# Kernel optimization log

Measured on AMD Instinct MI355X. Metric: run time of the kernel, lower is better.

## Reference

```python
import jax, jax.numpy as jnp
import numpy as np

TEMPERATURE = 0.1
EPS = 1e-12  # matches torch F.normalize default eps


def setup_inputs() -> dict:
    key = jax.random.key(0)
    k1, k2 = jax.random.split(key)
    B, D = 4096, 512
    features1 = jax.random.normal(k1, (B, D), dtype=jnp.float32)
    features2 = jax.random.normal(k2, (B, D), dtype=jnp.float32)
    return {"features1": features1, "features2": features2}


def _l2_normalize(x, axis=1):
    norm = jnp.linalg.norm(x, axis=axis, keepdims=True)
    return x / jnp.maximum(norm, EPS)


def reference(features1, features2):
    B = features1.shape[0]
    f1 = _l2_normalize(features1)
    f2 = _l2_normalize(features2)
    features = jnp.concatenate([f1, f2], axis=0)  # (2B, D)
    sim = jnp.matmul(features, features.T) / TEMPERATURE  # (2B, 2B)
    # mask self-similarity on the diagonal with -inf
    diag = jnp.eye(2 * B, dtype=bool)
    sim = jnp.where(diag, -jnp.inf, sim)
    # positive pair labels: row i pairs with i+B (first half) / i-B (second half)
    labels = jnp.concatenate([jnp.arange(B) + B, jnp.arange(B)], axis=0)
    log_probs = jax.nn.log_softmax(sim, axis=-1)  # (2B, 2B)
    nll = -jnp.take_along_axis(log_probs, labels[:, None], axis=1)[:, 0]
    return jnp.mean(nll)
```

## Files before the change

kernel.cpp:

```cpp
#include <hip/hip_runtime.h>

#define NROWS 8192
#define HALF_N 4096
#define DIM 512
#define INV_T 10.0f
#define NRB 64
#define NBLOCKS 2080

typedef __attribute__((ext_vector_type(4))) float f32x4;
typedef __attribute__((ext_vector_type(2))) long long2v;

__device__ __forceinline__ void async16(const void* g, void* l) {
  __builtin_amdgcn_global_load_lds(
      (const __attribute__((address_space(1))) unsigned int*)g,
      (__attribute__((address_space(3))) unsigned int*)l, 16, 0, 0);
}

__global__ __launch_bounds__(256) void norm_cast_k(
    const float* __restrict__ f1, const float* __restrict__ f2,
    unsigned char* __restrict__ Fa, unsigned char* __restrict__ Fb,
    float* __restrict__ rowsum, float* __restrict__ out) {
  int wave = threadIdx.x >> 6;
  int lane = threadIdx.x & 63;
  int row = blockIdx.x * 4 + wave;
  const float* src = (row < HALF_N) ? (f1 + (size_t)row * DIM)
                                    : (f2 + (size_t)(row - HALF_N) * DIM);
  const float4* p = reinterpret_cast<const float4*>(src + lane * 8);
  float4 v0 = p[0];
  float4 v1 = p[1];
  float ss = v0.x*v0.x + v0.y*v0.y + v0.z*v0.z + v0.w*v0.w
           + v1.x*v1.x + v1.y*v1.y + v1.z*v1.z + v1.w*v1.w;
  #pragma unroll
  for (int off = 1; off < 64; off <<= 1) ss += __shfl_xor(ss, off);
  float scale = 1.0f / fmaxf(sqrtf(ss), 1e-12f);
  int lo = __builtin_amdgcn_cvt_pk_fp8_f32(v0.x * scale, v0.y * scale, 0, false);
  lo = __builtin_amdgcn_cvt_pk_fp8_f32(v0.z * scale, v0.w * scale, lo, true);
  int hi = __builtin_amdgcn_cvt_pk_fp8_f32(v1.x * scale, v1.y * scale, 0, false);
  hi = __builtin_amdgcn_cvt_pk_fp8_f32(v1.z * scale, v1.w * scale, hi, true);
  int2 val = make_int2(lo, hi);
  int u = lane & 7;
  int g = lane >> 3;
  int pos = 2 * (u & 3) + (u >> 2);
  *reinterpret_cast<int2*>(Fb + (size_t)row * DIM + g * 64 + pos * 8) = val;
  int chunk = g * 4 + (u & 3);
  int slot = u >> 2;
  *reinterpret_cast<int2*>(Fa + (size_t)(row >> 4) * 8192 + chunk * 256 +
                           (row & 15) * 16 + slot * 8) = val;
  if (lane == 0) rowsum[row] = 0.0f;
  if (blockIdx.x == 0 && threadIdx.x == 0) out[0] = 0.0f;
}

__global__ __launch_bounds__(256, 3) void sym_gemm_k(
    const unsigned char* __restrict__ Fa, const unsigned char* __restrict__ Fb,
    float* __restrict__ rowsum, float* __restrict__ pairsim) {
  int bx = blockIdx.x;
  int gbx = (bx & 7) * (NBLOCKS / 8) + (bx >> 3);
  int rb = 0, rem = gbx;
  while (rem >= NRB - rb) { rem -= NRB - rb; ++rb; }
  const int cb = rb + rem;
  const int row0 = rb * 128, col0 = cb * 128;

  const int tid = threadIdx.x;
  const int wave = tid >> 6;
  const int lane = tid & 63;
  const int quad = lane >> 4;
  const int colid = lane & 15;
  const int wr0 = (wave >> 1) * 64;
  const int wc0 = (wave & 1) * 64;

  __shared__ __align__(16) unsigned char Blds[128 * 64];
  __shared__ float redrow[128];
  __shared__ float redcol[128];

  if (tid < 128) { redrow[tid] = 0.0f; redcol[tid] = 0.0f; }

  const unsigned char* srcB[2]; unsigned char* dstB[2];
  #pragma unroll
  for (int seg = 0; seg < 2; ++seg) {
    int inst = wave + seg * 4;
    int r = inst * 16 + (lane >> 2);
    int c = (lane & 3) ^ ((r >> 1) & 3);
    srcB[seg] = Fb + (size_t)(col0 + r) * DIM + c * 16;
    dstB[seg] = Blds + inst * 1024;
  }

  const unsigned char* agp[4];
  #pragma unroll
  for (int t = 0; t < 4; ++t)
    agp[t] = Fa + (size_t)((row0 + wr0 + t * 16) >> 4) * 8192 +
             quad * 256 + colid * 16;

  const unsigned char* bfp[4];
  #pragma unroll
  for (int t = 0; t < 4; ++t) {
    int rc = wc0 + t * 16 + colid;
    bfp[t] = Blds + rc * 64 + ((quad ^ ((rc >> 1) & 3)) << 4);
  }

  f32x4 acc[4][4];
  #pragma unroll
  for (int t = 0; t < 4; ++t)
    #pragma unroll
    for (int u = 0; u < 4; ++u) acc[t][u] = (f32x4){0.f, 0.f, 0.f, 0.f};

  for (int kc = 0; kc < 8; ++kc) {
    __syncthreads();
    const size_t ko = (size_t)kc * 64;
    #pragma unroll
    for (int seg = 0; seg < 2; ++seg)
      async16(srcB[seg] + ko, dstB[seg]);
    long2v af[4];
    #pragma unroll
    for (int t = 0; t < 4; ++t)
      af[t] = *reinterpret_cast<const long2v*>(agp[t] + kc * 1024);
    __syncthreads();

    long2v bf[4];
    #pragma unroll
    for (int u = 0; u < 4; ++u) bf[u] = *reinterpret_cast<const long2v*>(bfp[u]);
    #pragma unroll
    for (int s = 0; s < 2; ++s)
      #pragma unroll
      for (int t = 0; t < 4; ++t)
        #pragma unroll
        for (int u = 0; u < 4; ++u)
          acc[t][u] = __builtin_amdgcn_mfma_f32_16x16x32_fp8_fp8(
              af[t][s], bf[u][s], acc[t][u], 0, 0, 0);
  }

  float re[4][4];
  float ce[4];
  #pragma unroll
  for (int t = 0; t < 4; ++t)
    #pragma unroll
    for (int r = 0; r < 4; ++r) re[t][r] = 0.0f;
  #pragma unroll
  for (int u = 0; u < 4; ++u) ce[u] = 0.0f;

  #pragma unroll
  for (int t = 0; t < 4; ++t) {
    #pragma unroll
    for (int u = 0; u < 4; ++u) {
      f32x4 a = acc[t][u];
      const int gc = col0 + wc0 + u * 16 + colid;
      #pragma unroll
      for (int r = 0; r < 4; ++r) {
        int grow = row0 + wr0 + t * 16 + quad * 4 + r;
        float sim = a[r] * INV_T;
        float e = (gc > grow) ? __expf(sim) : 0.0f;
        re[t][r] += e;
        ce[u] += e;
        if (gc == grow + HALF_N && grow < HALF_N) {
          pairsim[grow] = sim;
          pairsim[gc] = sim;
        }
      }
    }
  }

  #pragma unroll
  for (int t = 0; t < 4; ++t)
    #pragma unroll
    for (int r = 0; r < 4; ++r) {
      float v = re[t][r];
      v += __shfl_xor(v, 1); v += __shfl_xor(v, 2);
      v += __shfl_xor(v, 4); v += __shfl_xor(v, 8);
      if (colid == 0) atomicAdd(&redrow[wr0 + t * 16 + quad * 4 + r], v);
    }
  #pragma unroll
  for (int u = 0; u < 4; ++u) {
    float v = ce[u];
    v += __shfl_xor(v, 16); v += __shfl_xor(v, 32);
    if (lane < 16) atomicAdd(&redcol[wc0 + u * 16 + colid], v);
  }
  __syncthreads();
  if (tid < 128) atomicAdd(&rowsum[row0 + tid], redrow[tid]);
  else           atomicAdd(&rowsum[col0 + tid - 128], redcol[tid - 128]);
}

__global__ __launch_bounds__(256) void finalize_k(
    const float* __restrict__ rowsum, const float* __restrict__ pairsim,
    float* __restrict__ out) {
  int i = blockIdx.x * 256 + threadIdx.x;
  float local = logf(rowsum[i]) - pairsim[i];
  #pragma unroll
  for (int off = 1; off < 64; off <<= 1) local += __shfl_xor(local, off);
  if ((threadIdx.x & 63) == 0)
    atomicAdd(out, local * (1.0f / (float)NROWS));
}

extern "C" void kernel_launch(void* const* d_in, const int* in_sizes, int n_in,
                              void* d_out, int out_size, void* d_ws, size_t ws_size,
                              hipStream_t stream) {
  const float* f1 = (const float*)d_in[0];
  const float* f2 = (const float*)d_in[1];
  unsigned char* Fa = (unsigned char*)d_ws;
  unsigned char* Fb = Fa + (size_t)NROWS * DIM;
  float* rowsum = (float*)(Fb + (size_t)NROWS * DIM);
  float* pairsim = rowsum + NROWS;
  float* out = (float*)d_out;

  norm_cast_k<<<NROWS / 4, 256, 0, stream>>>(f1, f2, Fa, Fb, rowsum, out);
  sym_gemm_k<<<NBLOCKS, 256, 0, stream>>>(Fa, Fb, rowsum, pairsim);
  finalize_k<<<NROWS / 256, 256, 0, stream>>>(rowsum, pairsim, out);
}
```

Measured before the change: 104.2 us.

## Load both GEMM operands directly from global into registers with double buffering

```diff
diff --git a/kernel.cpp b/kernel.cpp
--- a/kernel.cpp
+++ b/kernel.cpp
@@ -10,16 +10,10 @@
 typedef __attribute__((ext_vector_type(4))) float f32x4;
 typedef __attribute__((ext_vector_type(2))) long long2v;
 
-__device__ __forceinline__ void async16(const void* g, void* l) {
-  __builtin_amdgcn_global_load_lds(
-      (const __attribute__((address_space(1))) unsigned int*)g,
-      (__attribute__((address_space(3))) unsigned int*)l, 16, 0, 0);
-}
-
 __global__ __launch_bounds__(256) void norm_cast_k(
     const float* __restrict__ f1, const float* __restrict__ f2,
-    unsigned char* __restrict__ Fa, unsigned char* __restrict__ Fb,
-    float* __restrict__ rowsum, float* __restrict__ out) {
+    unsigned char* __restrict__ Fa, float* __restrict__ rowsum,
+    float* __restrict__ out) {
   int wave = threadIdx.x >> 6;
   int lane = threadIdx.x & 63;
   int row = blockIdx.x * 4 + wave;
@@ -37,22 +31,19 @@
   lo = __builtin_amdgcn_cvt_pk_fp8_f32(v0.z * scale, v0.w * scale, lo, true);
   int hi = __builtin_amdgcn_cvt_pk_fp8_f32(v1.x * scale, v1.y * scale, 0, false);
   hi = __builtin_amdgcn_cvt_pk_fp8_f32(v1.z * scale, v1.w * scale, hi, true);
-  int2 val = make_int2(lo, hi);
   int u = lane & 7;
   int g = lane >> 3;
-  int pos = 2 * (u & 3) + (u >> 2);
-  *reinterpret_cast<int2*>(Fb + (size_t)row * DIM + g * 64 + pos * 8) = val;
   int chunk = g * 4 + (u & 3);
   int slot = u >> 2;
   *reinterpret_cast<int2*>(Fa + (size_t)(row >> 4) * 8192 + chunk * 256 +
-                           (row & 15) * 16 + slot * 8) = val;
+                           (row & 15) * 16 + slot * 8) = make_int2(lo, hi);
   if (lane == 0) rowsum[row] = 0.0f;
   if (blockIdx.x == 0 && threadIdx.x == 0) out[0] = 0.0f;
 }
 
 __global__ __launch_bounds__(256, 3) void sym_gemm_k(
-    const unsigned char* __restrict__ Fa, const unsigned char* __restrict__ Fb,
-    float* __restrict__ rowsum, float* __restrict__ pairsim) {
+    const unsigned char* __restrict__ Fa, float* __restrict__ rowsum,
+    float* __restrict__ pairsim) {
   int bx = blockIdx.x;
   int gbx = (bx & 7) * (NBLOCKS / 8) + (bx >> 3);
   int rb = 0, rem = gbx;
@@ -68,33 +59,18 @@
   const int wr0 = (wave >> 1) * 64;
   const int wc0 = (wave & 1) * 64;
 
-  __shared__ __align__(16) unsigned char Blds[128 * 64];
   __shared__ float redrow[128];
   __shared__ float redcol[128];
+  if (tid < 128) { redrow[tid] = 0.0f; redcol[tid] = 0.0f; }
+  __syncthreads();
 
-  if (tid < 128) { redrow[tid] = 0.0f; redcol[tid] = 0.0f; }
-
-  const unsigned char* srcB[2]; unsigned char* dstB[2];
+  const unsigned char* agp[4]; const unsigned char* bgp[4];
   #pragma unroll
-  for (int seg = 0; seg < 2; ++seg) {
-    int inst = wave + seg * 4;
-    int r = inst * 16 + (lane >> 2);
-    int c = (lane & 3) ^ ((r >> 1) & 3);
-    srcB[seg] = Fb + (size_t)(col0 + r) * DIM + c * 16;
-    dstB[seg] = Blds + inst * 1024;
-  }
-
-  const unsigned char* agp[4];
-  #pragma unroll
-  for (int t = 0; t < 4; ++t)
+  for (int t = 0; t < 4; ++t) {
     agp[t] = Fa + (size_t)((row0 + wr0 + t * 16) >> 4) * 8192 +
              quad * 256 + colid * 16;
-
-  const unsigned char* bfp[4];
-  #pragma unroll
-  for (int t = 0; t < 4; ++t) {
-    int rc = wc0 + t * 16 + colid;
-    bfp[t] = Blds + rc * 64 + ((quad ^ ((rc >> 1) & 3)) << 4);
+    bgp[t] = Fa + (size_t)((col0 + wc0 + t * 16) >> 4) * 8192 +
+             quad * 256 + colid * 16;
   }
 
   f32x4 acc[4][4];
@@ -103,21 +79,23 @@
     #pragma unroll
     for (int u = 0; u < 4; ++u) acc[t][u] = (f32x4){0.f, 0.f, 0.f, 0.f};
 
+  long2v af[2][4], bf[2][4];
+  #pragma unroll
+  for (int t = 0; t < 4; ++t) {
+    af[0][t] = *reinterpret_cast<const long2v*>(agp[t]);
+    bf[0][t] = *reinterpret_cast<const long2v*>(bgp[t]);
+  }
+  #pragma unroll
   for (int kc = 0; kc < 8; ++kc) {
-    __syncthreads();
-    const size_t ko = (size_t)kc * 64;
-    #pragma unroll
-    for (int seg = 0; seg < 2; ++seg)
-      async16(srcB[seg] + ko, dstB[seg]);
-    long2v af[4];
-    #pragma unroll
-    for (int t = 0; t < 4; ++t)
-      af[t] = *reinterpret_cast<const long2v*>(agp[t] + kc * 1024);
-    __syncthreads();
-
-    long2v bf[4];
-    #pragma unroll
-    for (int u = 0; u < 4; ++u) bf[u] = *reinterpret_cast<const long2v*>(bfp[u]);
+    const int cur = kc & 1, nxt = cur ^ 1;
+    if (kc < 7) {
+      const int ko = (kc + 1) * 1024;
+      #pragma unroll
+      for (int t = 0; t < 4; ++t) {
+        af[nxt][t] = *reinterpret_cast<const long2v*>(agp[t] + ko);
+        bf[nxt][t] = *reinterpret_cast<const long2v*>(bgp[t] + ko);
+      }
+    }
     #pragma unroll
     for (int s = 0; s < 2; ++s)
       #pragma unroll
@@ -125,7 +103,7 @@
         #pragma unroll
         for (int u = 0; u < 4; ++u)
           acc[t][u] = __builtin_amdgcn_mfma_f32_16x16x32_fp8_fp8(
-              af[t][s], bf[u][s], acc[t][u], 0, 0, 0);
+              af[cur][t][s], bf[cur][u][s], acc[t][u], 0, 0, 0);
   }
 
   float re[4][4];
@@ -195,12 +173,11 @@
   const float* f1 = (const float*)d_in[0];
   const float* f2 = (const float*)d_in[1];
   unsigned char* Fa = (unsigned char*)d_ws;
-  unsigned char* Fb = Fa + (size_t)NROWS * DIM;
-  float* rowsum = (float*)(Fb + (size_t)NROWS * DIM);
+  float* rowsum = (float*)(Fa + (size_t)NROWS * DIM);
   float* pairsim = rowsum + NROWS;
   float* out = (float*)d_out;
 
-  norm_cast_k<<<NROWS / 4, 256, 0, stream>>>(f1, f2, Fa, Fb, rowsum, out);
-  sym_gemm_k<<<NBLOCKS, 256, 0, stream>>>(Fa, Fb, rowsum, pairsim);
+  norm_cast_k<<<NROWS / 4, 256, 0, stream>>>(f1, f2, Fa, rowsum, out);
+  sym_gemm_k<<<NBLOCKS, 256, 0, stream>>>(Fa, rowsum, pairsim);
   finalize_k<<<NROWS / 256, 256, 0, stream>>>(rowsum, pairsim, out);
 }
```

Measured after the change: 107.8 us. +3.5%, slower.

## Switch similarity GEMM from fp8 to int8 MFMA with fixed scale quantization

Applied to the files above, without the earlier changes.

```diff
diff --git a/kernel.cpp b/kernel.cpp
--- a/kernel.cpp
+++ b/kernel.cpp
@@ -3,17 +3,24 @@
 #define NROWS 8192
 #define HALF_N 4096
 #define DIM 512
-#define INV_T 10.0f
 #define NRB 64
 #define NBLOCKS 2080
+#define QS 423.3333333f
+#define SIMSCALE 5.5800111e-5f
 
 typedef __attribute__((ext_vector_type(4))) float f32x4;
-typedef __attribute__((ext_vector_type(2))) long long2v;
+typedef __attribute__((ext_vector_type(4))) int i32x4;
 
 __device__ __forceinline__ void async16(const void* g, void* l) {
   __builtin_amdgcn_global_load_lds(
       (const __attribute__((address_space(1))) unsigned int*)g,
       (__attribute__((address_space(3))) unsigned int*)l, 16, 0, 0);
+}
+
+__device__ __forceinline__ int pack4(float a, float b, float c, float d) {
+  int q0 = __float2int_rn(a), q1 = __float2int_rn(b);
+  int q2 = __float2int_rn(c), q3 = __float2int_rn(d);
+  return (q0 & 255) | ((q1 & 255) << 8) | ((q2 & 255) << 16) | (q3 << 24);
 }
 
 __global__ __launch_bounds__(256) void norm_cast_k(
@@ -32,18 +39,13 @@
            + v1.x*v1.x + v1.y*v1.y + v1.z*v1.z + v1.w*v1.w;
   #pragma unroll
   for (int off = 1; off < 64; off <<= 1) ss += __shfl_xor(ss, off);
-  float scale = 1.0f / fmaxf(sqrtf(ss), 1e-12f);
-  int lo = __builtin_amdgcn_cvt_pk_fp8_f32(v0.x * scale, v0.y * scale, 0, false);
-  lo = __builtin_amdgcn_cvt_pk_fp8_f32(v0.z * scale, v0.w * scale, lo, true);
-  int hi = __builtin_amdgcn_cvt_pk_fp8_f32(v1.x * scale, v1.y * scale, 0, false);
-  hi = __builtin_amdgcn_cvt_pk_fp8_f32(v1.z * scale, v1.w * scale, hi, true);
+  float sc = QS / fmaxf(sqrtf(ss), 1e-12f);
+  int lo = pack4(v0.x * sc, v0.y * sc, v0.z * sc, v0.w * sc);
+  int hi = pack4(v1.x * sc, v1.y * sc, v1.z * sc, v1.w * sc);
   int2 val = make_int2(lo, hi);
-  int u = lane & 7;
-  int g = lane >> 3;
-  int pos = 2 * (u & 3) + (u >> 2);
-  *reinterpret_cast<int2*>(Fb + (size_t)row * DIM + g * 64 + pos * 8) = val;
-  int chunk = g * 4 + (u & 3);
-  int slot = u >> 2;
+  *reinterpret_cast<int2*>(Fb + (size_t)row * DIM + lane * 8) = val;
+  int chunk = lane >> 1;
+  int slot = lane & 1;
   *reinterpret_cast<int2*>(Fa + (size_t)(row >> 4) * 8192 + chunk * 256 +
                            (row & 15) * 16 + slot * 8) = val;
   if (lane == 0) rowsum[row] = 0.0f;
@@ -71,7 +73,6 @@
   __shared__ __align__(16) unsigned char Blds[128 * 64];
   __shared__ float redrow[128];
   __shared__ float redcol[128];
-
   if (tid < 128) { redrow[tid] = 0.0f; redcol[tid] = 0.0f; }
 
   const unsigned char* srcB[2]; unsigned char* dstB[2];
@@ -97,11 +98,11 @@
     bfp[t] = Blds + rc * 64 + ((quad ^ ((rc >> 1) & 3)) << 4);
   }
 
-  f32x4 acc[4][4];
-  #pragma unroll
-  for (int t = 0; t < 4; ++t)
-    #pragma unroll
-    for (int u = 0; u < 4; ++u) acc[t][u] = (f32x4){0.f, 0.f, 0.f, 0.f};
+  i32x4 acc[4][4];
+  #pragma unroll
+  for (int t = 0; t < 4; ++t)
+    #pragma unroll
+    for (int u = 0; u < 4; ++u) acc[t][u] = (i32x4){0, 0, 0, 0};
 
   for (int kc = 0; kc < 8; ++kc) {
     __syncthreads();
@@ -109,23 +110,21 @@
     #pragma unroll
     for (int seg = 0; seg < 2; ++seg)
       async16(srcB[seg] + ko, dstB[seg]);
-    long2v af[4];
+    i32x4 af[4];
     #pragma unroll
     for (int t = 0; t < 4; ++t)
-      af[t] = *reinterpret_cast<const long2v*>(agp[t] + kc * 1024);
+      af[t] = *reinterpret_cast<const i32x4*>(agp[t] + kc * 1024);
     __syncthreads();
 
-    long2v bf[4];
-    #pragma unroll
-    for (int u = 0; u < 4; ++u) bf[u] = *reinterpret_cast<const long2v*>(bfp[u]);
-    #pragma unroll
-    for (int s = 0; s < 2; ++s)
+    i32x4 bf[4];
+    #pragma unroll
+    for (int u = 0; u < 4; ++u) bf[u] = *reinterpret_cast<const i32x4*>(bfp[u]);
+    #pragma unroll
+    for (int t = 0; t < 4; ++t)
       #pragma unroll
-      for (int t = 0; t < 4; ++t)
-        #pragma unroll
-        for (int u = 0; u < 4; ++u)
-          acc[t][u] = __builtin_amdgcn_mfma_f32_16x16x32_fp8_fp8(
-              af[t][s], bf[u][s], acc[t][u], 0, 0, 0);
+      for (int u = 0; u < 4; ++u)
+        acc[t][u] = __builtin_amdgcn_mfma_i32_16x16x64_i8(
+            af[t], bf[u], acc[t][u], 0, 0, 0);
   }
 
   float re[4][4];
@@ -141,12 +140,12 @@
   for (int t = 0; t < 4; ++t) {
     #pragma unroll
     for (int u = 0; u < 4; ++u) {
-      f32x4 a = acc[t][u];
+      i32x4 a = acc[t][u];
       const int gc = col0 + wc0 + u * 16 + colid;
       #pragma unroll
       for (int r = 0; r < 4; ++r) {
         int grow = row0 + wr0 + t * 16 + quad * 4 + r;
-        float sim = a[r] * INV_T;
+        float sim = (float)a[r] * SIMSCALE;
         float e = (gc > grow) ? __expf(sim) : 0.0f;
         re[t][r] += e;
         ce[u] += e;
```

After: 107.0 us. +2.7%, slower.
